# Optimization experiments

Measured on AMD Instinct MI355X. Metric: run time of the kernel, lower is better.

Reference implementation:

```python
import jax, jax.numpy as jnp
import numpy as np

DEPTH, HEADS, DIM_HEAD, DIM = 6, 16, 64, 1024
INNER = HEADS * DIM_HEAD  # 1024 == DIM
MLP = DIM                 # mlp_dim chosen == dim (see shape_source)
SCALE = DIM_HEAD ** -0.5
EPS = 1e-5


def _layernorm(x, w, b):
    m = jnp.mean(x, axis=-1, keepdims=True)
    v = jnp.mean(jnp.square(x - m), axis=-1, keepdims=True)
    return (x - m) * jax.lax.rsqrt(v + EPS) * w + b


def _rpq_weight(cb, codes):
    # cb: [G, 256, sub], codes: [out, G] -> W: [out, G*sub] == [out, in]
    G = cb.shape[0]
    W = cb[jnp.arange(G)[None, :], codes]  # [out, G, sub]
    return W.reshape(codes.shape[0], -1)


def _rpq_linear(x, cb, codes, b=None):
    W = _rpq_weight(cb, codes)
    y = jnp.einsum('bni,oi->bno', x, W)
    return y if b is None else y + b


def setup_inputs() -> dict:
    key = jax.random.key(0)
    ks = jax.random.split(key, 17)
    cs = 0.02  # codebook scale (kaiming-uniform-ish magnitude)
    return {
        'x': jax.random.normal(ks[0], (8, 1024, DIM), jnp.float32),
        'cb0': jax.random.normal(ks[1], (HEADS, 256, DIM // HEADS), jnp.float32) * cs,
        'cb1': jax.random.normal(ks[2], (HEADS, 256, DIM // HEADS), jnp.float32) * cs,
        'cb2': jax.random.normal(ks[3], (HEADS, 256, MLP // HEADS), jnp.float32) * cs,
        'cb3': jax.random.normal(ks[4], (HEADS, 256, MLP // HEADS), jnp.float32) * cs,
        'codes_qkv': jax.random.randint(ks[5], (DEPTH, 3 * INNER, HEADS), 0, 256, jnp.int32),
        'codes_out': jax.random.randint(ks[6], (DEPTH, DIM, HEADS), 0, 256, jnp.int32),
        'codes_fc1': jax.random.randint(ks[7], (DEPTH, MLP, HEADS), 0, 256, jnp.int32),
        'codes_fc2': jax.random.randint(ks[8], (DEPTH, DIM, HEADS), 0, 256, jnp.int32),
        'b_out': jax.random.normal(ks[9], (DEPTH, DIM), jnp.float32) * 0.02,
        'b_fc1': jax.random.normal(ks[10], (DEPTH, MLP), jnp.float32) * 0.02,
        'b_fc2': jax.random.normal(ks[11], (DEPTH, DIM), jnp.float32) * 0.02,
        'ln1_w': jax.random.uniform(ks[12], (DEPTH, DIM), jnp.float32, 0.5, 1.5),
        'ln1_b': jax.random.normal(ks[13], (DEPTH, DIM), jnp.float32) * 0.02,
        'ln2_w': jax.random.uniform(ks[14], (DEPTH, DIM), jnp.float32, 0.5, 1.5),
        'ln2_b': jax.random.normal(ks[15], (DEPTH, DIM), jnp.float32) * 0.02,
    }


def reference(x, cb0, cb1, cb2, cb3, codes_qkv, codes_out, codes_fc1, codes_fc2,
              b_out, b_fc1, b_fc2, ln1_w, ln1_b, ln2_w, ln2_b):
    b, n, _ = x.shape
    for i in range(DEPTH):
        # PreNorm Attention
        xn = _layernorm(x, ln1_w[i], ln1_b[i])
        qkv = _rpq_linear(xn, cb0, codes_qkv[i])  # [b, n, 3*INNER]
        q, k, v = jnp.split(qkv, 3, axis=-1)
        q = q.reshape(b, n, HEADS, DIM_HEAD).transpose(0, 2, 1, 3)  # bhnd
        k = k.reshape(b, n, HEADS, DIM_HEAD).transpose(0, 2, 1, 3)
        v = v.reshape(b, n, HEADS, DIM_HEAD).transpose(0, 2, 1, 3)
        dots = jnp.einsum('bhqd,bhkd->bhqk', q, k) * SCALE
        attn = jax.nn.softmax(dots, axis=-1)
        out = jnp.einsum('bhqk,bhkd->bhqd', attn, v)
        out = out.transpose(0, 2, 1, 3).reshape(b, n, INNER)
        out = _rpq_linear(out, cb1, codes_out[i], b_out[i])
        x = out + x
        # PreNorm FeedForward
        xn = _layernorm(x, ln2_w[i], ln2_b[i])
        h = jax.nn.gelu(_rpq_linear(xn, cb2, codes_fc1[i], b_fc1[i]), approximate=False)
        x = _rpq_linear(h, cb3, codes_fc2[i], b_fc2[i]) + x
    return x
```

## Files before the change

kernel.cpp:

```cpp
#include <hip/hip_runtime.h>
#include <hip/hip_bf16.h>


typedef __bf16 bf16x8 __attribute__((ext_vector_type(8)));
typedef __bf16 bf16x4 __attribute__((ext_vector_type(4)));
typedef float  f32x4  __attribute__((ext_vector_type(4)));
typedef float  f32x16 __attribute__((ext_vector_type(16)));
typedef unsigned int u32x4 __attribute__((ext_vector_type(4)));
typedef unsigned int u32_as1 __attribute__((address_space(1)));
typedef unsigned int u32_as3 __attribute__((address_space(3)));

#define MFMA16(a, b, c) __builtin_amdgcn_mfma_f32_16x16x32_bf16(a, b, c, 0, 0, 0)
#define MFMA32(a, b, c) __builtin_amdgcn_mfma_f32_32x32x16_bf16(a, b, c, 0, 0, 0)

__device__ __forceinline__ void gload16(void* lds, const void* g) {
  __builtin_amdgcn_global_load_lds((u32_as1*)(void*)g, (u32_as3*)lds, 16, 0, 0);
}

__device__ __forceinline__ unsigned pack2(float a, float b) {
  unsigned lo = (unsigned)__builtin_bit_cast(unsigned short, (__bf16)a);
  unsigned hi = (unsigned)__builtin_bit_cast(unsigned short, (__bf16)b);
  return lo | (hi << 16);
}
__device__ __forceinline__ void pswap(unsigned& a, unsigned& b) {
  asm("v_permlane32_swap_b32 %0, %1" : "+v"(a), "+v"(b));
}

__device__ __forceinline__ int xcd_swizzle(int orig, int nwg) {
  const int xcd = orig & 7, idx = orig >> 3;
  const int q = nwg >> 3, r = nwg & 7;
  return (xcd < r ? xcd * (q + 1) : r * (q + 1) + (xcd - r) * q) + idx;
}

__global__ __launch_bounds__(256) void dequant_kernel(
    __bf16* __restrict__ W,
    const float* __restrict__ cb0, const float* __restrict__ cb1,
    const float* __restrict__ cb2, const float* __restrict__ cb3,
    const int* __restrict__ codes_qkv, const int* __restrict__ codes_out,
    const int* __restrict__ codes_fc1, const int* __restrict__ codes_fc2)
{
  const int r = blockIdx.x;
  const int t = threadIdx.x;
  const float* cb; const int* cr;
  if (r < 3072)      { cb = cb0; cr = codes_qkv + r * 16; }
  else if (r < 4096) { cb = cb1; cr = codes_out + (r - 3072) * 16; }
  else if (r < 5120) { cb = cb2; cr = codes_fc1 + (r - 4096) * 16; }
  else               { cb = cb3; cr = codes_fc2 + (r - 5120) * 16; }
  const int g = t >> 4, j = (t & 15) * 4;
  const int code = cr[g];
  const float4 v = *(const float4*)(cb + ((size_t)(g * 256 + code) * 64) + j);
  bf16x4 o = { (__bf16)v.x, (__bf16)v.y, (__bf16)v.z, (__bf16)v.w };
  *(bf16x4*)(W + (size_t)r * 1024 + g * 64 + j) = o;
}

__global__ __launch_bounds__(256) void ln_kernel(
    const float* __restrict__ x, const float* __restrict__ w,
    const float* __restrict__ b, __bf16* __restrict__ out)
{
  const int row = blockIdx.x, t = threadIdx.x;
  const float4 v = *(const float4*)(x + (size_t)row * 1024 + t * 4);
  float s  = v.x + v.y + v.z + v.w;
  float sq = v.x * v.x + v.y * v.y + v.z * v.z + v.w * v.w;
  #pragma unroll
  for (int off = 32; off > 0; off >>= 1) {
    s  += __shfl_xor(s,  off, 64);
    sq += __shfl_xor(sq, off, 64);
  }
  __shared__ float red[8];
  const int wid = t >> 6, lane = t & 63;
  if (lane == 0) { red[wid] = s; red[4 + wid] = sq; }
  __syncthreads();
  s  = red[0] + red[1] + red[2] + red[3];
  sq = red[4] + red[5] + red[6] + red[7];
  const float mean = s * (1.0f / 1024.0f);
  const float var  = sq * (1.0f / 1024.0f) - mean * mean;
  const float rstd = rsqrtf(var + 1e-5f);
  const float4 wv = *(const float4*)(w + t * 4);
  const float4 bv = *(const float4*)(b + t * 4);
  bf16x4 o = { (__bf16)((v.x - mean) * rstd * wv.x + bv.x),
               (__bf16)((v.y - mean) * rstd * wv.y + bv.y),
               (__bf16)((v.z - mean) * rstd * wv.z + bv.z),
               (__bf16)((v.w - mean) * rstd * wv.w + bv.w) };
  *(bf16x4*)(out + (size_t)row * 1024 + t * 4) = o;
}

template<int EPI>
__global__ __launch_bounds__(256) void gemm_kernel(
    const __bf16* __restrict__ A, const __bf16* __restrict__ Bw,
    __bf16* __restrict__ oQ, __bf16* __restrict__ oK, __bf16* __restrict__ oVT,
    __bf16* __restrict__ oH, float* __restrict__ oX, const float* __restrict__ bias,
    int nTiles)
{
  __shared__ char smem[32768] __attribute__((aligned(128)));
  const int tid  = threadIdx.x;
  const int lane = tid & 63, wid = tid >> 6;
  const int l15 = lane & 15, l4 = lane >> 4;
  const int wr = wid >> 1, wc = wid & 1;
  const int wgid = xcd_swizzle(blockIdx.x, gridDim.x);
  const int m0 = (wgid / nTiles) * 128, n0 = (wgid % nTiles) * 128;

  const int srow8 = lane >> 3;
  const int scole = (lane & 7) * 8;

  f32x4 acc[4][4];
  #pragma unroll
  for (int i = 0; i < 4; ++i)
    #pragma unroll
    for (int j = 0; j < 4; ++j) acc[i][j] = (f32x4){0.f, 0.f, 0.f, 0.f};

  const __bf16* gA = A  + (size_t)(m0 + srow8) * 1024 + scole;
  const __bf16* gB = Bw + (size_t)(n0 + srow8) * 1024 + scole;

  for (int kk = 0; kk < 16; ++kk) {
    const int kb = kk * 64;
    #pragma unroll
    for (int ii = 0; ii < 4; ++ii) {
      const int chunk = wid * 4 + ii;
      gload16(smem + chunk * 1024,         gA + (size_t)chunk * 8192 + kb);
      gload16(smem + 16384 + chunk * 1024, gB + (size_t)chunk * 8192 + kb);
    }
    __syncthreads();
    #pragma unroll
    for (int ks = 0; ks < 2; ++ks) {
      bf16x8 af[4], bfr[4];
      #pragma unroll
      for (int mi = 0; mi < 4; ++mi)
        af[mi] = *(const bf16x8*)(smem + (wr * 64 + mi * 16 + l15) * 128 + ks * 64 + l4 * 16);
      #pragma unroll
      for (int ni = 0; ni < 4; ++ni)
        bfr[ni] = *(const bf16x8*)(smem + 16384 + (wc * 64 + ni * 16 + l15) * 128 + ks * 64 + l4 * 16);
      #pragma unroll
      for (int mi = 0; mi < 4; ++mi)
        #pragma unroll
        for (int ni = 0; ni < 4; ++ni)
          acc[mi][ni] = MFMA16(af[mi], bfr[ni], acc[mi][ni]);
    }
    __syncthreads();
  }

  #pragma unroll
  for (int mi = 0; mi < 4; ++mi) {
    #pragma unroll
    for (int ni = 0; ni < 4; ++ni) {
      const int n = n0 + wc * 64 + ni * 16 + l15;
      if constexpr (EPI == 0) {
        const int region = n >> 10, nn = n & 1023;
        const int hh = nn >> 6, d = nn & 63;
        const int m_base = m0 + wr * 64 + mi * 16 + l4 * 4;
        const int bb = m_base >> 10, s = m_base & 1023;
        if (region == 2) {
          bf16x4 pv = { (__bf16)acc[mi][ni][0], (__bf16)acc[mi][ni][1],
                        (__bf16)acc[mi][ni][2], (__bf16)acc[mi][ni][3] };
          *(bf16x4*)(oVT + ((size_t)(bb * 16 + hh) * 64 + d) * 1024 + s) = pv;
        } else {
          #pragma unroll
          for (int r = 0; r < 4; ++r) {
            const __bf16 bv = (__bf16)acc[mi][ni][r];
            if (region == 0) oQ[((size_t)(bb * 16 + hh) * 1024 + s + r) * 64 + d] = bv;
            else             oK[((size_t)(bb * 16 + hh) * 1024 + s + r) * 64 + d] = bv;
          }
        }
      } else {
        #pragma unroll
        for (int r = 0; r < 4; ++r) {
          const int m = m0 + wr * 64 + mi * 16 + l4 * 4 + r;
          const float v = acc[mi][ni][r];
          if constexpr (EPI == 1) {
            float* p = oX + (size_t)m * 1024 + n;
            *p = *p + v + bias[n];
          } else {
            float t = v + bias[n];
            t = 0.5f * t * (1.0f + erff(t * 0.70710678118f));
            oH[(size_t)m * 1024 + n] = (__bf16)t;
          }
        }
      }
    }
  }
}

__global__ __launch_bounds__(512, 4) void attn_kernel(
    const __bf16* __restrict__ Q, const __bf16* __restrict__ K,
    const __bf16* __restrict__ VT, __bf16* __restrict__ AO)
{
  const int bh = blockIdx.x & 127;
  const int qt = blockIdx.x >> 7;
  const int tid = threadIdx.x, lane = tid & 63, wid = tid >> 6;
  const int l31 = lane & 31, hi = lane >> 5;
  const int q0 = qt * 256 + wid * 32;

  const __bf16* Qb = Q  + (size_t)bh * 65536;
  const __bf16* Kb = K  + (size_t)bh * 65536;
  const __bf16* Vb = VT + (size_t)bh * 65536;

  __shared__ char lds[2][16384] __attribute__((aligned(128)));

  const float ascale = 0.125f * 1.44269504089f;

  const int srow_in_chunk = lane >> 3;
  const int scol = (((lane & 7) ^ srow_in_chunk ^ (wid & 3)) << 3);

  #define STAGE(buf, kb_)                                                       \
    {                                                                           \
      const int row_ = wid * 8 + srow_in_chunk;                                 \
      gload16((buf) + wid * 1024, Kb + (size_t)((kb_) + row_) * 64 + scol);     \
      gload16((buf) + 8192 + wid * 1024, Vb + (size_t)row_ * 1024 + (kb_) + scol); \
    }

  bf16x8 qf[4];
  #pragma unroll
  for (int c = 0; c < 4; ++c)
    qf[c] = *(const bf16x8*)(Qb + (size_t)(q0 + l31) * 64 + c * 16 + hi * 8);

  const u32x4 onesu = { 0x3f803f80u, 0x3f803f80u, 0x3f803f80u, 0x3f803f80u };
  const bf16x8 ones = __builtin_bit_cast(bf16x8, onesu);

  f32x16 o0, o1, sacc;
  #pragma unroll
  for (int r = 0; r < 16; ++r) { o0[r] = 0.f; o1[r] = 0.f; sacc[r] = 0.f; }
  float m = -1e30f;

  const int swz = (((l31 & 7) ^ ((l31 >> 3) & 3)) << 4);

  STAGE(lds[0], 0);

  for (int kt = 0; kt < 16; ++kt) {
    __syncthreads();
    const char* Kl = lds[kt & 1];
    const char* Vl = lds[kt & 1] + 8192;
    if (kt < 15) STAGE(lds[(kt + 1) & 1], (kt + 1) * 64);

    f32x16 s0, s1;
    #pragma unroll
    for (int r = 0; r < 16; ++r) { s0[r] = 0.f; s1[r] = 0.f; }
    __builtin_amdgcn_s_setprio(1);
    #pragma unroll
    for (int c = 0; c < 4; ++c) {
      bf16x8 kf0 = *(const bf16x8*)(Kl + l31 * 128        + ((c * 32 + hi * 16) ^ swz));
      bf16x8 kf1 = *(const bf16x8*)(Kl + (32 + l31) * 128 + ((c * 32 + hi * 16) ^ swz));
      s0 = MFMA32(kf0, qf[c], s0);
      s1 = MFMA32(kf1, qf[c], s1);
    }
    __builtin_amdgcn_s_setprio(0);
    float t0 = fmaxf(s0[0], s0[1]),  t1 = fmaxf(s0[2], s0[3]);
    float t2 = fmaxf(s0[4], s0[5]),  t3 = fmaxf(s0[6], s0[7]);
    float t4 = fmaxf(s0[8], s0[9]),  t5 = fmaxf(s0[10], s0[11]);
    float t6 = fmaxf(s0[12], s0[13]), t7 = fmaxf(s0[14], s0[15]);
    float u0 = fmaxf(s1[0], s1[1]),  u1 = fmaxf(s1[2], s1[3]);
    float u2 = fmaxf(s1[4], s1[5]),  u3 = fmaxf(s1[6], s1[7]);
    float u4 = fmaxf(s1[8], s1[9]),  u5 = fmaxf(s1[10], s1[11]);
    float u6 = fmaxf(s1[12], s1[13]), u7 = fmaxf(s1[14], s1[15]);
    t0 = fmaxf(fmaxf(t0, t1), fmaxf(t2, t3));
    t4 = fmaxf(fmaxf(t4, t5), fmaxf(t6, t7));
    u0 = fmaxf(fmaxf(u0, u1), fmaxf(u2, u3));
    u4 = fmaxf(fmaxf(u4, u5), fmaxf(u6, u7));
    float pm = fmaxf(fmaxf(t0, t4), fmaxf(u0, u4));
    pm = fmaxf(pm, __shfl_xor(pm, 32, 64));
    const float pmx = pm * ascale;
    if (__any((int)(pmx > m + 8.0f))) {
      const float mnew = fmaxf(m, pmx);
      const float a = exp2f(m - mnew);
      m = mnew;
      #pragma unroll
      for (int r = 0; r < 16; ++r) {
        const float ab = __shfl(a, (r & 3) + 8 * (r >> 2) + 4 * hi, 64);
        o0[r] *= ab; o1[r] *= ab; sacc[r] *= ab;
      }
    }
    const float nm = -m;
    #pragma unroll
    for (int r = 0; r < 16; ++r) {
      s0[r] = exp2f(fmaf(s0[r], ascale, nm));
      s1[r] = exp2f(fmaf(s1[r], ascale, nm));
    }
    unsigned a0 = pack2(s0[0], s0[1]),   b0 = pack2(s0[4], s0[5]);
    unsigned a1 = pack2(s0[2], s0[3]),   b1 = pack2(s0[6], s0[7]);
    unsigned a2 = pack2(s0[8], s0[9]),   b2 = pack2(s0[12], s0[13]);
    unsigned a3 = pack2(s0[10], s0[11]), b3 = pack2(s0[14], s0[15]);
    unsigned c0 = pack2(s1[0], s1[1]),   d0 = pack2(s1[4], s1[5]);
    unsigned c1 = pack2(s1[2], s1[3]),   d1 = pack2(s1[6], s1[7]);
    unsigned c2 = pack2(s1[8], s1[9]),   d2 = pack2(s1[12], s1[13]);
    unsigned c3 = pack2(s1[10], s1[11]), d3 = pack2(s1[14], s1[15]);
    pswap(a0, b0); pswap(a1, b1); pswap(a2, b2); pswap(a3, b3);
    pswap(c0, d0); pswap(c1, d1); pswap(c2, d2); pswap(c3, d3);
    bf16x8 pfrag[4];
    pfrag[0] = __builtin_bit_cast(bf16x8, (u32x4){a0, a1, b0, b1});
    pfrag[1] = __builtin_bit_cast(bf16x8, (u32x4){a2, a3, b2, b3});
    pfrag[2] = __builtin_bit_cast(bf16x8, (u32x4){c0, c1, d0, d1});
    pfrag[3] = __builtin_bit_cast(bf16x8, (u32x4){c2, c3, d2, d3});
    __builtin_amdgcn_s_setprio(1);
    #pragma unroll
    for (int c = 0; c < 4; ++c) {
      bf16x8 v0 = *(const bf16x8*)(Vl + l31 * 128        + ((c * 32 + hi * 16) ^ swz));
      bf16x8 v1 = *(const bf16x8*)(Vl + (32 + l31) * 128 + ((c * 32 + hi * 16) ^ swz));
      o0 = MFMA32(pfrag[c], v0, o0);
      o1 = MFMA32(pfrag[c], v1, o1);
      sacc = MFMA32(pfrag[c], ones, sacc);
    }
    __builtin_amdgcn_s_setprio(0);
  }
  #undef STAGE

  const int bb = bh >> 4, hh = bh & 15;
  #pragma unroll
  for (int r = 0; r < 16; ++r) {
    const int crow = (r & 3) + 8 * (r >> 2) + 4 * hi;
    const float lb = 1.0f / sacc[r];
    const int srow = q0 + crow;
    AO[(size_t)(bb * 1024 + srow) * 1024 + hh * 64 + l31]      = (__bf16)(o0[r] * lb);
    AO[(size_t)(bb * 1024 + srow) * 1024 + hh * 64 + 32 + l31] = (__bf16)(o1[r] * lb);
  }
}

extern "C" void kernel_launch(void* const* d_in, const int* in_sizes, int n_in,
                              void* d_out, int out_size, void* d_ws, size_t ws_size,
                              hipStream_t stream)
{
  const float* x        = (const float*)d_in[0];
  const float* cb0      = (const float*)d_in[1];
  const float* cb1      = (const float*)d_in[2];
  const float* cb2      = (const float*)d_in[3];
  const float* cb3      = (const float*)d_in[4];
  const int* codes_qkv  = (const int*)d_in[5];
  const int* codes_out  = (const int*)d_in[6];
  const int* codes_fc1  = (const int*)d_in[7];
  const int* codes_fc2  = (const int*)d_in[8];
  const float* b_out    = (const float*)d_in[9];
  const float* b_fc1    = (const float*)d_in[10];
  const float* b_fc2    = (const float*)d_in[11];
  const float* ln1_w    = (const float*)d_in[12];
  const float* ln1_b    = (const float*)d_in[13];
  const float* ln2_w    = (const float*)d_in[14];
  const float* ln2_b    = (const float*)d_in[15];

  float* X = (float*)d_out;
  __bf16* ws = (__bf16*)d_ws;
  __bf16* W  = ws;
  __bf16* xn = ws + 6291456;
  __bf16* Qb = ws + 14680064;
  __bf16* Kb = ws + 23068672;
  __bf16* VT = ws + 31457280;
  __bf16* AO = ws + 39845888;
  __bf16* Hb = ws + 48234496;

  hipMemcpyAsync(X, x, (size_t)8192 * 1024 * 4, hipMemcpyDeviceToDevice, stream);

  for (int i = 0; i < 6; ++i) {
    dequant_kernel<<<6144, 256, 0, stream>>>(
        W, cb0, cb1, cb2, cb3,
        codes_qkv + (size_t)i * 3072 * 16, codes_out + (size_t)i * 1024 * 16,
        codes_fc1 + (size_t)i * 1024 * 16, codes_fc2 + (size_t)i * 1024 * 16);

    ln_kernel<<<8192, 256, 0, stream>>>(X, ln1_w + i * 1024, ln1_b + i * 1024, xn);

    gemm_kernel<0><<<1536, 256, 0, stream>>>(
        xn, W, Qb, Kb, VT, nullptr, nullptr, nullptr, 24);

    attn_kernel<<<512, 512, 0, stream>>>(Qb, Kb, VT, AO);

    gemm_kernel<1><<<512, 256, 0, stream>>>(
        AO, W + (size_t)3072 * 1024, nullptr, nullptr, nullptr, nullptr, X, b_out + i * 1024, 8);

    ln_kernel<<<8192, 256, 0, stream>>>(X, ln2_w + i * 1024, ln2_b + i * 1024, xn);

    gemm_kernel<2><<<512, 256, 0, stream>>>(
        xn, W + (size_t)4096 * 1024, nullptr, nullptr, nullptr, Hb, nullptr, b_fc1 + i * 1024, 8);

    gemm_kernel<1><<<512, 256, 0, stream>>>(
        Hb, W + (size_t)5120 * 1024, nullptr, nullptr, nullptr, nullptr, X, b_fc2 + i * 1024, 8);
  }
}
```

Baseline: 1.592 ms.

## Double-buffer GEMM LDS tiles with K=32 stages and MFMA priority boost

```diff
diff --git a/kernel.cpp b/kernel.cpp
--- a/kernel.cpp
+++ b/kernel.cpp
@@ -91,7 +91,7 @@
     __bf16* __restrict__ oH, float* __restrict__ oX, const float* __restrict__ bias,
     int nTiles)
 {
-  __shared__ char smem[32768] __attribute__((aligned(128)));
+  __shared__ char smem[2][16384] __attribute__((aligned(128)));
   const int tid  = threadIdx.x;
   const int lane = tid & 63, wid = tid >> 6;
   const int l15 = lane & 15, l4 = lane >> 4;
@@ -99,8 +99,8 @@
   const int wgid = xcd_swizzle(blockIdx.x, gridDim.x);
   const int m0 = (wgid / nTiles) * 128, n0 = (wgid % nTiles) * 128;
 
-  const int srow8 = lane >> 3;
-  const int scole = (lane & 7) * 8;
+  const int srow = tid >> 2;
+  const int scol = (tid & 3) * 8;
 
   f32x4 acc[4][4];
   #pragma unroll
@@ -108,35 +108,42 @@
     #pragma unroll
     for (int j = 0; j < 4; ++j) acc[i][j] = (f32x4){0.f, 0.f, 0.f, 0.f};
 
-  const __bf16* gA = A  + (size_t)(m0 + srow8) * 1024 + scole;
-  const __bf16* gB = Bw + (size_t)(n0 + srow8) * 1024 + scole;
-
-  for (int kk = 0; kk < 16; ++kk) {
-    const int kb = kk * 64;
-    #pragma unroll
-    for (int ii = 0; ii < 4; ++ii) {
-      const int chunk = wid * 4 + ii;
-      gload16(smem + chunk * 1024,         gA + (size_t)chunk * 8192 + kb);
-      gload16(smem + 16384 + chunk * 1024, gB + (size_t)chunk * 8192 + kb);
-    }
+  const __bf16* gA = A  + (size_t)(m0 + srow) * 1024 + scol;
+  const __bf16* gB = Bw + (size_t)(n0 + srow) * 1024 + scol;
+  const int aoff = l15 * 64 + l4 * 16;
+
+  #define GSTAGE(buf, kb_)                                          \
+    {                                                               \
+      gload16((buf) + wid * 1024,         gA + (kb_));              \
+      gload16((buf) + 4096 + wid * 1024,  gA + 64 * 1024 + (kb_));  \
+      gload16((buf) + 8192 + wid * 1024,  gB + (kb_));              \
+      gload16((buf) + 12288 + wid * 1024, gB + 64 * 1024 + (kb_));  \
+    }
+
+  GSTAGE(smem[0], 0);
+
+  for (int kk = 0; kk < 32; ++kk) {
     __syncthreads();
-    #pragma unroll
-    for (int ks = 0; ks < 2; ++ks) {
-      bf16x8 af[4], bfr[4];
-      #pragma unroll
-      for (int mi = 0; mi < 4; ++mi)
-        af[mi] = *(const bf16x8*)(smem + (wr * 64 + mi * 16 + l15) * 128 + ks * 64 + l4 * 16);
+    const char* sA = smem[kk & 1];
+    const char* sB = sA + 8192;
+    if (kk < 31) GSTAGE(smem[(kk + 1) & 1], (kk + 1) * 32);
+
+    bf16x8 af[4], bfr[4];
+    #pragma unroll
+    for (int mi = 0; mi < 4; ++mi)
+      af[mi] = *(const bf16x8*)(sA + (wr * 64 + mi * 16) * 64 + aoff);
+    #pragma unroll
+    for (int ni = 0; ni < 4; ++ni)
+      bfr[ni] = *(const bf16x8*)(sB + (wc * 64 + ni * 16) * 64 + aoff);
+    __builtin_amdgcn_s_setprio(1);
+    #pragma unroll
+    for (int mi = 0; mi < 4; ++mi)
       #pragma unroll
       for (int ni = 0; ni < 4; ++ni)
-        bfr[ni] = *(const bf16x8*)(smem + 16384 + (wc * 64 + ni * 16 + l15) * 128 + ks * 64 + l4 * 16);
-      #pragma unroll
-      for (int mi = 0; mi < 4; ++mi)
-        #pragma unroll
-        for (int ni = 0; ni < 4; ++ni)
-          acc[mi][ni] = MFMA16(af[mi], bfr[ni], acc[mi][ni]);
-    }
-    __syncthreads();
-  }
+        acc[mi][ni] = MFMA16(af[mi], bfr[ni], acc[mi][ni]);
+    __builtin_amdgcn_s_setprio(0);
+  }
+  #undef GSTAGE
 
   #pragma unroll
   for (int mi = 0; mi < 4; ++mi) {
```

Measured after the change: 1.658 ms. 4.1% more time.
